# Performance work log

Hardware: AMD Instinct MI355X
Metric: run time of the kernel (lower is better)

The kernel has to match this reference:

```python
import jax, jax.numpy as jnp
import numpy as np

DIM = 384; KEY_DIM = 32; HEADS = 8; ATTN_RATIO = 4; RES = 14
D = ATTN_RATIO * KEY_DIM          # 128
DH = D * HEADS                    # 1024
QK = HEADS * KEY_DIM              # 256
B = 64
EPS = 1e-5
SCALE = KEY_DIM ** -0.5


def _bn(x, p):
    # inference-mode BatchNorm; p = [gamma, beta, mean, var] each [C]; channel axis = 1
    g, b, m, v = p
    shp = (1, -1) + (1,) * (x.ndim - 2)
    return (x - m.reshape(shp)) * jax.lax.rsqrt(v.reshape(shp) + EPS) * g.reshape(shp) + b.reshape(shp)


def _bn_params(k, c):
    k1, k2, k3, k4 = jax.random.split(k, 4)
    gamma = 1.0 + 0.1 * jax.random.normal(k1, (c,), dtype=jnp.float32)
    beta = 0.02 * jax.random.normal(k2, (c,), dtype=jnp.float32)
    mean = 0.1 * jax.random.normal(k3, (c,), dtype=jnp.float32)
    var = jax.random.uniform(k4, (c,), dtype=jnp.float32) + 0.5
    return jnp.stack([gamma, beta, mean, var])


def setup_inputs() -> dict:
    key = jax.random.key(0)
    ks = jax.random.split(key, 24)
    def rn(i, shape, s=0.05):
        return s * jax.random.normal(ks[i], shape, dtype=jnp.float32)
    # relative-position bias index table: offset (|dy|,|dx|) -> dy*RES+dx
    coords = np.stack(np.meshgrid(np.arange(RES), np.arange(RES), indexing='ij'), -1).reshape(-1, 2)
    off = np.abs(coords[:, None, :] - coords[None, :, :])  # [N,N,2]
    bias_idxs = jnp.asarray(off[..., 0] * RES + off[..., 1], dtype=jnp.int32)  # [N,N]
    return {
        'x': jax.random.normal(ks[0], (B, DIM, RES, RES), dtype=jnp.float32),
        'wq': rn(1, (QK, DIM)), 'bq': rn(2, (QK,)), 'bnq': _bn_params(ks[3], QK),
        'wk': rn(4, (QK, DIM)), 'bk': rn(5, (QK,)), 'bnk': _bn_params(ks[6], QK),
        'wv': rn(7, (DH, DIM)), 'bv': rn(8, (DH,)), 'bnv': _bn_params(ks[9], DH),
        'wvl': rn(10, (DH, 1, 3, 3)), 'bvl': rn(11, (DH,)), 'bnvl': _bn_params(ks[12], DH),
        'th1w': rn(13, (HEADS, HEADS), 0.2), 'th1b': rn(14, (HEADS,)),
        'th2w': rn(15, (HEADS, HEADS), 0.2), 'th2b': rn(16, (HEADS,)),
        'wp': rn(17, (DIM, DH)), 'bp': rn(18, (DIM,)), 'bnp': _bn_params(ks[19], DIM),
        'ab': rn(20, (HEADS, RES * RES), 0.1),
        'bias_idxs': bias_idxs,
    }


def reference(x, wq, bq, bnq, wk, bk, bnk, wv, bv, bnv, wvl, bvl, bnvl,
              th1w, th1b, th2w, th2b, wp, bp, bnp, ab, bias_idxs):
    Bn, C, H, W = x.shape
    N = H * W
    xf = x.reshape(Bn, C, N)
    # 1x1 conv + BN branches (channel GEMMs)
    q = _bn(jnp.einsum('oc,bcn->bon', wq, xf) + bq[None, :, None], bnq)
    k = _bn(jnp.einsum('oc,bcn->bon', wk, xf) + bk[None, :, None], bnk)
    v = _bn(jnp.einsum('oc,bcn->bon', wv, xf) + bv[None, :, None], bnv)  # [B,DH,N]
    # local value path: 3x3 depthwise conv + BN
    v_img = v.reshape(Bn, DH, H, W)
    v_local = jax.lax.conv_general_dilated(
        v_img, wvl, window_strides=(1, 1), padding='SAME',
        feature_group_count=DH, dimension_numbers=('NCHW', 'OIHW', 'NCHW'))
    v_local = _bn(v_local + bvl[None, :, None, None], bnvl)
    # attention
    qh = q.reshape(Bn, HEADS, KEY_DIM, N).transpose(0, 1, 3, 2)  # b h n d
    kh = k.reshape(Bn, HEADS, KEY_DIM, N)                        # b h d m
    vh = v.reshape(Bn, HEADS, D, N).transpose(0, 1, 3, 2)        # b h m e
    attn = jnp.einsum('bhnd,bhdm->bhnm', qh, kh) * SCALE
    attn = attn + ab[:, bias_idxs][None]                         # [1,H,N,N] positional bias
    attn = jnp.einsum('oh,bhnm->bonm', th1w, attn) + th1b[None, :, None, None]
    attn = jax.nn.softmax(attn, axis=-1)
    attn = jnp.einsum('oh,bhnm->bonm', th2w, attn) + th2b[None, :, None, None]
    out = jnp.einsum('bhnm,bhme->bhne', attn, vh)                # b h n e
    out = out.transpose(0, 1, 3, 2).reshape(Bn, DH, H, W) + v_local
    # proj: ReLU -> 1x1 conv -> BN
    out = jax.nn.relu(out)
    out = jnp.einsum('oc,bchw->bohw', wp, out) + bp[None, :, None, None]
    return _bn(out, bnp)
```

## Files before the change

kernel.cpp:

```cpp
#include <hip/hip_runtime.h>

#define B_     64
#define DIM_   384
#define RES_   14
#define N_     196
#define HEADS_ 8
#define KD_    32
#define D_     128
#define DH_    1024
#define QK_    256
#define CH_    1536
#define EPS_   1e-5f
#define SCALE_ 0.17677669529663687f

typedef unsigned short u16;
typedef unsigned int u32;
typedef short v8s __attribute__((ext_vector_type(8)));
typedef float v4f __attribute__((ext_vector_type(4)));
typedef u16  v4u __attribute__((ext_vector_type(4)));
typedef u32  v2u __attribute__((ext_vector_type(2)));
typedef _Float16 h2 __attribute__((ext_vector_type(2)));

static __device__ __forceinline__ u16 f2bf(float f) {
    unsigned int u = __builtin_bit_cast(unsigned int, f);
    u = (u + 0x7fffu + ((u >> 16) & 1u)) >> 16;
    return (u16)u;
}
static __device__ __forceinline__ float bf2f(u16 u) {
    unsigned int x = ((unsigned int)u) << 16;
    return __builtin_bit_cast(float, x);
}

#define WBI_OFF  0u
#define WPI_OFF  589824u
#define QI_OFF   983040u
#define KI_OFF   5177344u
#define VI_OFF   9371648u
#define VLOC_U16 53411840u
#define TAIL_OFF 79101952u
#define TB_OFF   98770944u
#define BIASE_OFF 98785920u

template<int KSTEPS>
static __device__ __forceinline__ void gemm_direct(
    const u16* __restrict__ Ag, const u16* __restrict__ Bg,
    v4f acc[4][4], int tid)
{
    const int lane = tid & 63, w = tid >> 6;
    const int wm = (w & 1) * 64, wn = (w >> 1) * 64;
    const int quad = lane >> 4, l16 = lane & 15;
    const u16* pa = Ag + quad * 1024 + (wm + l16) * 8;
    const u16* pb = Bg + quad * 1024 + (wn + l16) * 8;
    v8s a[2][4], b[2][4];
    #pragma unroll
    for (int i = 0; i < 4; i++) {
        a[0][i] = *(const v8s*)(pa + i * 128);
        b[0][i] = *(const v8s*)(pb + i * 128);
    }
    #pragma unroll
    for (int ks = 0; ks < KSTEPS; ks++) {
        const int cur = ks & 1, nxt = cur ^ 1;
        if (ks + 1 < KSTEPS) {
            const u16* qa = pa + (size_t)(ks + 1) * 4096;
            const u16* qb = pb + (size_t)(ks + 1) * 4096;
            #pragma unroll
            for (int i = 0; i < 4; i++) {
                a[nxt][i] = *(const v8s*)(qa + i * 128);
                b[nxt][i] = *(const v8s*)(qb + i * 128);
            }
        }
        #pragma unroll
        for (int i = 0; i < 4; i++)
            #pragma unroll
            for (int j = 0; j < 4; j++)
                acc[i][j] = __builtin_amdgcn_mfma_f32_16x16x32_bf16(a[cur][i], b[cur][j], acc[i][j], 0, 0, 0);
    }
}

template<int KSTEPS>
static __device__ __forceinline__ void gemm_direct3(
    const u16* __restrict__ Ag, const u16* __restrict__ Bg,
    v4f acc[4][4], int tid)
{
    const int lane = tid & 63, w = tid >> 6;
    const int wm = (w & 1) * 64, wn = (w >> 1) * 64;
    const int quad = lane >> 4, l16 = lane & 15;
    const u16* pa = Ag + quad * 1024 + (wm + l16) * 8;
    const u16* pb = Bg + quad * 1024 + (wn + l16) * 8;
    v8s a[3][4], b[3][4];
    #pragma unroll
    for (int s = 0; s < 2; s++) {
        #pragma unroll
        for (int i = 0; i < 4; i++) {
            a[s][i] = *(const v8s*)(pa + (size_t)s * 4096 + i * 128);
            b[s][i] = *(const v8s*)(pb + (size_t)s * 4096 + i * 128);
        }
    }
    #pragma unroll
    for (int ks = 0; ks < KSTEPS; ks++) {
        const int cur = ks % 3, nxt = (ks + 2) % 3;
        if (ks + 2 < KSTEPS) {
            const u16* qa = pa + (size_t)(ks + 2) * 4096;
            const u16* qb = pb + (size_t)(ks + 2) * 4096;
            #pragma unroll
            for (int i = 0; i < 4; i++) {
                a[nxt][i] = *(const v8s*)(qa + i * 128);
                b[nxt][i] = *(const v8s*)(qb + i * 128);
            }
        }
        #pragma unroll
        for (int i = 0; i < 4; i++)
            #pragma unroll
            for (int j = 0; j < 4; j++)
                acc[i][j] = __builtin_amdgcn_mfma_f32_16x16x32_bf16(a[cur][i], b[cur][j], acc[i][j], 0, 0, 0);
    }
}

__global__ __launch_bounds__(256) void k_pre(
    const float* __restrict__ x,
    const float* __restrict__ wq, const float* __restrict__ wk,
    const float* __restrict__ wv, const float* __restrict__ wp,
    const float* __restrict__ ab,
    const float* __restrict__ th1w, const float* __restrict__ th1b,
    const float* __restrict__ bq, const float* __restrict__ bnq,
    const float* __restrict__ bk, const float* __restrict__ bnk,
    const float* __restrict__ bv, const float* __restrict__ bnv,
    const float* __restrict__ bp, const float* __restrict__ bnp,
    const float* __restrict__ bvl, const float* __restrict__ bnvl,
    const int* __restrict__ bidx,
    u16* __restrict__ xI, u16* __restrict__ WbI, u16* __restrict__ WpI,
    float* __restrict__ TB, float* __restrict__ biasE)
{
    __shared__ float T[64][65];
    const int tid = threadIdx.x;
    if (blockIdx.x < 1536) {
        const int t  = blockIdx.x;
        const int n0 = (t & 3) * 64;
        const int k0 = ((t >> 2) % 6) * 64;
        const int b  = t / 24;
        const int c = tid & 63, r4 = tid >> 6;
        #pragma unroll
        for (int i = 0; i < 16; i++) {
            int kr = i * 4 + r4;
            int gn = n0 + c;
            T[kr][c] = (gn < N_) ? x[((size_t)b * DIM_ + k0 + kr) * N_ + gn] : 0.f;
        }
        __syncthreads();
        #pragma unroll
        for (int it = 0; it < 16; it++) {
            int j = it * 256 + tid;
            int kk = j & 63, nn = j >> 6;
            int k = k0 + kk, n = n0 + nn;
            xI[(size_t)b * 98304 + (n >> 7) * 49152 + (k >> 5) * 4096
               + ((k >> 3) & 3) * 1024 + (n & 127) * 8 + (k & 7)] = f2bf(T[kk][nn]);
        }
        return;
    }
    int i = (blockIdx.x - 1536) * 256 + tid;
    if (i < 589824) {
        int mt = i / 49152, rem = i % 49152;
        int ks = rem >> 12, r2 = rem & 4095;
        int q = r2 >> 10, row = (r2 >> 3) & 127, e = r2 & 7;
        int c = mt * 128 + row, k = ks * 32 + q * 8 + e;
        float v = (c < 256) ? wq[c * 384 + k]
                : (c < 512) ? wk[(c - 256) * 384 + k]
                            : wv[(size_t)(c - 512) * 384 + k];
        WbI[i] = f2bf(v);
    } else if (i < 983040) {
        int j = i - 589824;
        int mt = j >> 17, rem = j & 131071;
        int ks = rem >> 12, r2 = rem & 4095;
        int q = r2 >> 10, row = (r2 >> 3) & 127, e = r2 & 7;
        int p = mt * 128 + row, k = ks * 32 + q * 8 + e;
        WpI[j] = f2bf(wp[(size_t)p * 1024 + k]);
    } else if (i < 985984) {
        int j = i - 983040;
        if (j < 256) {
            int c = j;
            float s = bnq[c] * rsqrtf(bnq[768 + c] + EPS_);
            float t = (bq[c] - bnq[512 + c]) * s + bnq[256 + c];
            TB[c] = s * SCALE_; TB[256 + c] = t * SCALE_;
        } else if (j < 512) {
            int c = j - 256;
            float s = bnk[c] * rsqrtf(bnk[768 + c] + EPS_);
            float t = (bk[c] - bnk[512 + c]) * s + bnk[256 + c];
            TB[512 + c] = s; TB[768 + c] = t;
        } else if (j < 1536) {
            int c = j - 512;
            float s = bnv[c] * rsqrtf(bnv[3072 + c] + EPS_);
            float t = (bv[c] - bnv[2048 + c]) * s + bnv[1024 + c];
            TB[1024 + c] = s; TB[2048 + c] = t;
        } else if (j < 1920) {
            int c = j - 1536;
            float s = bnp[c] * rsqrtf(bnp[1152 + c] + EPS_);
            float t = (bp[c] - bnp[768 + c]) * s + bnp[384 + c];
            TB[3072 + c] = s; TB[3456 + c] = t;
        } else {
            int c = j - 1920;
            float s = bnvl[c] * rsqrtf(bnvl[3072 + c] + EPS_);
            float t = (bvl[c] - bnvl[2048 + c]) * s + bnvl[1024 + c];
            TB[3840 + c] = s; TB[4864 + c] = t;
        }
    } else if (i < 1293312) {
        int j = i - 985984;
        int m = j % N_;
        int t = j / N_;
        int o = t & 7;
        int n = t >> 3;
        int idx = bidx[n * N_ + m];
        float a = th1b[o];
        #pragma unroll
        for (int h = 0; h < 8; h++) a += th1w[o * 8 + h] * ab[h * N_ + idx];
        biasE[j] = a - 5.f;
    }
}

__global__ __launch_bounds__(256) void k_qkv(
    const u16* __restrict__ WbI, const u16* __restrict__ xI,
    const float* __restrict__ TB,
    u16* __restrict__ qI, u16* __restrict__ kI, u16* __restrict__ vI)
{
    const int tid = threadIdx.x;
    const int L = blockIdx.x + 2 * (blockIdx.y + 12 * blockIdx.z);
    const int idx = L >> 3;
    const int b  = (L & 7) * 8 + idx / 24;
    const int r  = idx % 24;
    const int mt = r >> 1, nt = r & 1;
    v4f acc[4][4] = {};
    gemm_direct<12>(WbI + (size_t)mt * 49152,
                    xI + ((size_t)b * 2 + nt) * 49152, acc, tid);

    const int lane = tid & 63, w = tid >> 6;
    const int wm = (w & 1) * 64, wn = (w >> 1) * 64;
    const int quad = lane >> 4, l16 = lane & 15;
    #pragma unroll
    for (int i = 0; i < 4; i++) {
        #pragma unroll
        for (int j = 0; j < 4; j++) {
            int gc = mt * 128 + wm + i * 16 + quad * 4;
            int n  = nt * 128 + wn + j * 16 + l16;
            v4f v = acc[i][j];
            if (gc < 256) {
                v4f s = *(const v4f*)&TB[gc];
                v4f t = *(const v4f*)&TB[256 + gc];
                v4u u;
                #pragma unroll
                for (int r2 = 0; r2 < 4; r2++) u[r2] = f2bf(v[r2] * s[r2] + t[r2]);
                *(v4u*)&qI[((size_t)(b * 8 + (gc >> 5)) * 256 + n) * 32 + (gc & 31)] = u;
            } else if (gc < 512) {
                int c = gc - 256;
                v4f s = *(const v4f*)&TB[512 + c];
                v4f t = *(const v4f*)&TB[768 + c];
                v4u u;
                #pragma unroll
                for (int r2 = 0; r2 < 4; r2++) u[r2] = f2bf(v[r2] * s[r2] + t[r2]);
                *(v4u*)&kI[((size_t)(b * 8 + (c >> 5)) * 256 + n) * 32 + (c & 31)] = u;
            } else {
                int c = gc - 512;
                if (n < 224) {
                    int o = c >> 7, e = c & 127;
                    u16* base = vI + ((size_t)(b * 8 + o) * 7 + (n >> 5)) * 4096
                                + ((n >> 3) & 3) * 1024 + (n & 7);
                    #pragma unroll
                    for (int r2 = 0; r2 < 4; r2++) {
                        u16 outv = 0;
                        if (n < N_) outv = f2bf(v[r2] * TB[1024 + c + r2] + TB[2048 + c + r2]);
                        base[(e + r2) * 8] = outv;
                    }
                }
            }
        }
    }
}

__global__ __launch_bounds__(256) void k_dwconv(
    const u16* __restrict__ vI, const float* __restrict__ wvl,
    const float* __restrict__ TB, u16* __restrict__ vlocI)
{
    __shared__ u16 V[64 * 230];
    const int tid = threadIdx.x;
    const int sub = blockIdx.x;
    const int b   = blockIdx.y;
    const int o   = sub >> 1;
    const int e0  = (sub & 1) * 64;
    const u16* img = vI + (size_t)(b * 8 + o) * 28672;

    {
        const int quad = tid >> 6, l = tid & 63;
        #pragma unroll
        for (int i = 0; i < 7; i++) {
            v8s u = *(const v8s*)&img[i * 4096 + quad * 1024 + (e0 + l) * 8];
            const u32* ui = (const u32*)&u;
            int m0 = i * 32 + quad * 8;
            u32* dst = (u32*)&V[l * 230 + m0];
            #pragma unroll
            for (int c = 0; c < 4; c++) dst[c] = ui[c];
        }
    }
    __syncthreads();

    const int e = tid & 63, j = tid >> 6;
    const int cg = sub * 64 + e;
    const int y0 = j * 4;
    const int ny = (j == 3) ? 2 : 4;
    float wgt[9];
    #pragma unroll
    for (int k = 0; k < 9; k++) wgt[k] = wvl[cg * 9 + k];
    const float sc = TB[3840 + cg], sh = TB[4864 + cg];
    u32 po[4][7];

    for (int yi = 0; yi < ny; yi++) {
        int y = y0 + yi;
        float a[3][16];
        #pragma unroll
        for (int dy = 0; dy < 3; dy++) {
            int yy = y + dy - 1;
            a[dy][0] = 0.f; a[dy][15] = 0.f;
            if (yy < 0 || yy > 13) {
                #pragma unroll
                for (int x = 1; x < 15; x++) a[dy][x] = 0.f;
            } else {
                const u16* rp = &V[e * 230 + yy * 14];
                #pragma unroll
                for (int c4 = 0; c4 < 7; c4++) {
                    u32 u = *(const u32*)&rp[c4 * 2];
                    a[dy][1 + 2 * c4] = bf2f((u16)(u & 0xffffu));
                    a[dy][2 + 2 * c4] = bf2f((u16)(u >> 16));
                }
            }
        }
        #pragma unroll
        for (int xp = 0; xp < 7; xp++) {
            u32 pk = 0;
            #pragma unroll
            for (int half = 0; half < 2; half++) {
                int x = 2 * xp + half;
                float s = 0.f;
                #pragma unroll
                for (int dy = 0; dy < 3; dy++)
                    #pragma unroll
                    for (int kx = 0; kx < 3; kx++)
                        s += wgt[dy * 3 + kx] * a[dy][x + kx];
                u16 bv = f2bf(s * sc + sh);
                pk |= ((u32)bv) << (16 * half);
            }
            po[yi][xp] = pk;
        }
    }
    __syncthreads();

    for (int yi = 0; yi < ny; yi++) {
        u32* dst = (u32*)&V[e * 196 + (y0 + yi) * 14];
        #pragma unroll
        for (int xp = 0; xp < 7; xp++) dst[xp] = po[yi][xp];
    }
    __syncthreads();

    for (int it = 0; it < 7; it++) {
        int idx = it * 256 + tid;
        if (idx < 1568) {
            int g = idx / 196, n = idx - g * 196;
            v4u lo, hi;
            #pragma unroll
            for (int r = 0; r < 4; r++) lo[r] = V[(g * 8 + r) * 196 + n];
            #pragma unroll
            for (int r = 0; r < 4; r++) hi[r] = V[(g * 8 + 4 + r) * 196 + n];
            u16* dst = vlocI + ((size_t)(b * 2 + (n >> 7)) * 32 + sub * 2 + (g >> 2)) * 4096
                     + (g & 3) * 1024 + (n & 127) * 8;
            *(v4u*)dst = lo;
            *(v4u*)(dst + 4) = hi;
        }
    }
}

#define SLST 232
__global__ __launch_bounds__(512, 4) void k_attn_av(
    const u16* __restrict__ qI, const u16* __restrict__ kI,
    const u16* __restrict__ vI,
    const float* __restrict__ th1w,
    const float* __restrict__ th2w, const float* __restrict__ th2b,
    const float* __restrict__ biasE,
    const u16* __restrict__ vlocI, u16* __restrict__ aoI)
{
    __shared__ __attribute__((aligned(16))) u16 Ps[2][16 * SLST];
    __shared__ float red[8][8][16];
    __shared__ float invS[8][16];
    __shared__ __attribute__((aligned(16))) u16 Zf[8];
    const int tid = threadIdx.x;
    const int w = tid >> 6, lane = tid & 63;
    const int quad = lane >> 4, l16 = lane & 15;
    const int L = blockIdx.x + 13 * blockIdx.y;
    const int idx = L >> 3;
    const int b  = (L & 7) * 8 + idx / 13;
    const int qt = idx % 13;
    const int n0 = qt * 16;
    if (tid < 8) Zf[tid] = 0;

    const int nmt = (w < 5) ? 2 : 1;
    const int nq  = n0 + l16;
    const int nb  = (nq < N_) ? nq : 0;
    const float* bErow = biasE + (size_t)nb * 1568;

    h2 E[2][8][2] = {};
    #pragma unroll
    for (int mi = 0; mi < 2; mi++) {
        if (mi >= nmt) break;
        const int mt = w + mi * 8;
        v4f S[8];
        const u16* qb0 = qI + (size_t)b * 8 * 8192;
        const u16* kb0 = kI + (size_t)b * 8 * 8192;
        #pragma unroll
        for (int h = 0; h < 8; h++) {
            v8s qf = *(const v8s*)&qb0[h * 8192 + (n0 + l16) * 32 + quad * 8];
            v8s kf = *(const v8s*)&kb0[h * 8192 + (mt * 16 + l16) * 32 + quad * 8];
            v4f z = {};
            S[h] = __builtin_amdgcn_mfma_f32_16x16x32_bf16(kf, qf, z, 0, 0, 0);
        }
        const bool mvalid = (mt < 12) || (quad == 0);
        const int mb = mt * 16 + quad * 4;
        if (mvalid) {
            #pragma unroll
            for (int o = 0; o < 8; o++) {
                v4f a = *(const v4f*)&bErow[o * 196 + mb];
                #pragma unroll
                for (int h = 0; h < 8; h++) {
                    float t1 = th1w[o * 8 + h];
                    #pragma unroll
                    for (int r = 0; r < 4; r++) a[r] += t1 * S[h][r];
                }
                E[mi][o][0] = h2{(_Float16)__expf(a[0]), (_Float16)__expf(a[1])};
                E[mi][o][1] = h2{(_Float16)__expf(a[2]), (_Float16)__expf(a[3])};
            }
        }
    }

    {
        float psum[8];
        #pragma unroll
        for (int o = 0; o < 8; o++) {
            float s = (float)E[0][o][0].x + (float)E[0][o][0].y
                    + (float)E[0][o][1].x + (float)E[0][o][1].y
                    + (float)E[1][o][0].x + (float)E[1][o][0].y
                    + (float)E[1][o][1].x + (float)E[1][o][1].y;
            s += __shfl_xor(s, 16, 64);
            s += __shfl_xor(s, 32, 64);
            psum[o] = s;
        }
        red[w][quad * 2 + 0][l16] = psum[quad * 2 + 0];
        red[w][quad * 2 + 1][l16] = psum[quad * 2 + 1];
    }
    __syncthreads();
    if (tid < 128) {
        int o = tid >> 4, q = tid & 15;
        float s = 0.f;
        #pragma unroll
        for (int wv = 0; wv < 8; wv++) s += red[wv][o][q];
        invS[o][q] = 1.f / s;
    }
    __syncthreads();

    #pragma unroll
    for (int o = 0; o < 8; o++) {
        float is = invS[o][l16];
        h2 is2 = h2{(_Float16)is, (_Float16)is};
        E[0][o][0] *= is2; E[0][o][1] *= is2;
        E[1][o][0] *= is2; E[1][o][1] *= is2;
    }

    const int half_ = n0 >> 7;
    const int row0 = n0 & 127;
    const bool act = (nq < N_);
    char* psrow0 = (char*)&Ps[0][0] + l16 * (SLST * 2);
    char* psrow1 = (char*)&Ps[1][0] + l16 * (SLST * 2);

    #pragma unroll
    for (int o2 = 0; o2 < 8; o2++) {
        char* psb = (o2 & 1) ? psrow1 : psrow0;
        #pragma unroll
        for (int mi = 0; mi < 2; mi++) {
            if (mi >= nmt) break;
            const int mt = w + mi * 8;
            const bool mvalid = (mt < 12) || (quad == 0);
            u32 pk0 = 0, pk1 = 0;
            if (mvalid) {
                float p0 = th2b[o2], p1 = th2b[o2], p2 = th2b[o2], p3 = th2b[o2];
                #pragma unroll
                for (int o = 0; o < 8; o++) {
                    float wgt = th2w[o2 * 8 + o];
                    p0 += wgt * (float)E[mi][o][0].x;
                    p1 += wgt * (float)E[mi][o][0].y;
                    p2 += wgt * (float)E[mi][o][1].x;
                    p3 += wgt * (float)E[mi][o][1].y;
                }
                pk0 = (u32)f2bf(p0) | ((u32)f2bf(p1) << 16);
                pk1 = (u32)f2bf(p2) | ((u32)f2bf(p3) << 16);
            }
            v2u pw; pw[0] = pk0; pw[1] = pk1;
            *(v2u*)(psb + mt * 32 + quad * 8) = pw;
        }
        const u16* vb = vI + (size_t)(b * 8 + o2) * 28672;
        const u16* af = vb + quad * 1024 + (w * 16 + l16) * 8;
        v8s va[7];
        #pragma unroll
        for (int ks = 0; ks < 7; ks++)
            va[ks] = *(const v8s*)(af + (size_t)ks * 4096);
        __syncthreads();

        v4f acc = {};
        __builtin_amdgcn_s_setprio(1);
        #pragma unroll
        for (int ks = 0; ks < 7; ks++) {
            v8s bfr = (ks == 6 && quad >= 2)
                    ? *(const v8s*)&Zf[0]
                    : *(const v8s*)(psb + ks * 64 + quad * 16);
            acc = __builtin_amdgcn_mfma_f32_16x16x32_bf16(va[ks], bfr, acc, 0, 0, 0);
        }
        __builtin_amdgcn_s_setprio(0);

        if (act) {
            const int c0 = o2 * 128 + w * 16 + quad * 4;
            const size_t ioff = ((size_t)(b * 2 + half_) * 32 + (c0 >> 5)) * 4096
                              + ((c0 >> 3) & 3) * 1024 + (size_t)(row0 + l16) * 8 + (c0 & 7);
            v4u lv = *(const v4u*)&vlocI[ioff];
            v4u u;
            #pragma unroll
            for (int r = 0; r < 4; r++)
                u[r] = f2bf(fmaxf(acc[r] + bf2f(lv[r]), 0.f));
            *(v4u*)&aoI[ioff] = u;
        }
    }
}

__global__ __launch_bounds__(256) void k_proj(
    const u16* __restrict__ WpI, const u16* __restrict__ aoI,
    const float* __restrict__ TB, float* __restrict__ out)
{
    const int tid = threadIdx.x;
    const int L = blockIdx.x + 2 * (blockIdx.y + 3 * blockIdx.z);
    const int idx = L >> 3;
    const int b  = (L & 7) * 8 + idx / 6;
    const int r  = idx % 6;
    const int mt = r >> 1, nt = r & 1;
    v4f acc[4][4] = {};
    gemm_direct3<32>(WpI + (size_t)mt * 131072,
                     aoI + ((size_t)b * 2 + nt) * 131072, acc, tid);

    const int lane = tid & 63, w = tid >> 6;
    const int wm = (w & 1) * 64, wn = (w >> 1) * 64;
    const int quad = lane >> 4, l16 = lane & 15;
    #pragma unroll
    for (int i = 0; i < 4; i++) {
        #pragma unroll
        for (int j = 0; j < 4; j++) {
            int p0 = mt * 128 + wm + i * 16 + quad * 4;
            int n  = nt * 128 + wn + j * 16 + l16;
            if (n < N_) {
                v4f s = *(const v4f*)&TB[3072 + p0];
                v4f t = *(const v4f*)&TB[3456 + p0];
                #pragma unroll
                for (int r2 = 0; r2 < 4; r2++)
                    out[((size_t)b * DIM_ + p0 + r2) * N_ + n] = acc[i][j][r2] * s[r2] + t[r2];
            }
        }
    }
}

extern "C" void kernel_launch(void* const* d_in, const int* in_sizes, int n_in,
                              void* d_out, int out_size, void* d_ws, size_t ws_size,
                              hipStream_t stream)
{
    const float* x    = (const float*)d_in[0];
    const float* wq   = (const float*)d_in[1];
    const float* bq   = (const float*)d_in[2];
    const float* bnq  = (const float*)d_in[3];
    const float* wk   = (const float*)d_in[4];
    const float* bk   = (const float*)d_in[5];
    const float* bnk  = (const float*)d_in[6];
    const float* wv   = (const float*)d_in[7];
    const float* bv   = (const float*)d_in[8];
    const float* bnv  = (const float*)d_in[9];
    const float* wvl  = (const float*)d_in[10];
    const float* bvl  = (const float*)d_in[11];
    const float* bnvl = (const float*)d_in[12];
    const float* th1w = (const float*)d_in[13];
    const float* th1b = (const float*)d_in[14];
    const float* th2w = (const float*)d_in[15];
    const float* th2b = (const float*)d_in[16];
    const float* wp   = (const float*)d_in[17];
    const float* bp   = (const float*)d_in[18];
    const float* bnp  = (const float*)d_in[19];
    const float* ab   = (const float*)d_in[20];
    const int*   bidx = (const int*)d_in[21];
    float* out = (float*)d_out;

    u16* wsb  = (u16*)d_ws;
    u16* WbI  = wsb + WBI_OFF;
    u16* WpI  = wsb + WPI_OFF;
    u16* qI   = wsb + QI_OFF;
    u16* kI   = wsb + KI_OFF;
    u16* vI   = wsb + VI_OFF;
    u16* vlocI = wsb + VLOC_U16;
    u16* xI   = wsb + TAIL_OFF;
    u16* aoI  = wsb + TAIL_OFF;
    float* TB    = (float*)(wsb + TB_OFF);
    float* biasE = (float*)(wsb + BIASE_OFF);

    k_pre<<<dim3(6588), 256, 0, stream>>>(x, wq, wk, wv, wp, ab, th1w, th1b,
                                          bq, bnq, bk, bnk, bv, bnv, bp, bnp, bvl, bnvl,
                                          bidx, xI, WbI, WpI, TB, biasE);
    k_qkv<<<dim3(2, 12, B_), 256, 0, stream>>>(WbI, xI, TB, qI, kI, vI);
    k_dwconv<<<dim3(16, B_), 256, 0, stream>>>(vI, wvl, TB, vlocI);
    k_attn_av<<<dim3(13, B_), 512, 0, stream>>>(qI, kI, vI, th1w, th2w, th2b,
                                                biasE, vlocI, aoI);
    k_proj<<<dim3(2, 3, B_), 256, 0, stream>>>(WpI, aoI, TB, out);
}
```

Baseline: 257.1 us.

## Fuse output projection GEMM into attention kernel via shared-memory staging

The separate k_proj launch is removed. Each attention block now stages its ReLU'd bf16 attention output tile (16 queries x 512 channels at a time) in swizzled LDS and multiplies it by Wp with MFMA, accumulating the 384 output channels in registers before applying the final BN affine and writing fp32 output. This drops the aoI round trip through global memory and one kernel launch. In exchange, every block reads all of Wp from global or L2 for only 16 query rows, adds two extra barriers, and uses more LDS and registers, which may reduce occupancy.

```diff
diff --git a/kernel.cpp b/kernel.cpp
--- a/kernel.cpp
+++ b/kernel.cpp
@@ -63,45 +63,6 @@
         if (ks + 1 < KSTEPS) {
             const u16* qa = pa + (size_t)(ks + 1) * 4096;
             const u16* qb = pb + (size_t)(ks + 1) * 4096;
-            #pragma unroll
-            for (int i = 0; i < 4; i++) {
-                a[nxt][i] = *(const v8s*)(qa + i * 128);
-                b[nxt][i] = *(const v8s*)(qb + i * 128);
-            }
-        }
-        #pragma unroll
-        for (int i = 0; i < 4; i++)
-            #pragma unroll
-            for (int j = 0; j < 4; j++)
-                acc[i][j] = __builtin_amdgcn_mfma_f32_16x16x32_bf16(a[cur][i], b[cur][j], acc[i][j], 0, 0, 0);
-    }
-}
-
-template<int KSTEPS>
-static __device__ __forceinline__ void gemm_direct3(
-    const u16* __restrict__ Ag, const u16* __restrict__ Bg,
-    v4f acc[4][4], int tid)
-{
-    const int lane = tid & 63, w = tid >> 6;
-    const int wm = (w & 1) * 64, wn = (w >> 1) * 64;
-    const int quad = lane >> 4, l16 = lane & 15;
-    const u16* pa = Ag + quad * 1024 + (wm + l16) * 8;
-    const u16* pb = Bg + quad * 1024 + (wn + l16) * 8;
-    v8s a[3][4], b[3][4];
-    #pragma unroll
-    for (int s = 0; s < 2; s++) {
-        #pragma unroll
-        for (int i = 0; i < 4; i++) {
-            a[s][i] = *(const v8s*)(pa + (size_t)s * 4096 + i * 128);
-            b[s][i] = *(const v8s*)(pb + (size_t)s * 4096 + i * 128);
-        }
-    }
-    #pragma unroll
-    for (int ks = 0; ks < KSTEPS; ks++) {
-        const int cur = ks % 3, nxt = (ks + 2) % 3;
-        if (ks + 2 < KSTEPS) {
-            const u16* qa = pa + (size_t)(ks + 2) * 4096;
-            const u16* qb = pb + (size_t)(ks + 2) * 4096;
             #pragma unroll
             for (int i = 0; i < 4; i++) {
                 a[nxt][i] = *(const v8s*)(qa + i * 128);
@@ -380,12 +341,15 @@
     const float* __restrict__ th1w,
     const float* __restrict__ th2w, const float* __restrict__ th2b,
     const float* __restrict__ biasE,
-    const u16* __restrict__ vlocI, u16* __restrict__ aoI)
+    const u16* __restrict__ vlocI,
+    const u16* __restrict__ WpI, const float* __restrict__ TB,
+    float* __restrict__ out)
 {
     __shared__ __attribute__((aligned(16))) u16 Ps[2][16 * SLST];
-    __shared__ float red[8][8][16];
-    __shared__ float invS[8][16];
+    __shared__ __attribute__((aligned(16))) u16 Ao[16 * 512];
     __shared__ __attribute__((aligned(16))) u16 Zf[8];
+    float* red  = (float*)&Ao[0];
+    float* invS = (float*)&Ao[2048];
     const int tid = threadIdx.x;
     const int w = tid >> 6, lane = tid & 63;
     const int quad = lane >> 4, l16 = lane & 15;
@@ -446,32 +410,34 @@
             s += __shfl_xor(s, 32, 64);
             psum[o] = s;
         }
-        red[w][quad * 2 + 0][l16] = psum[quad * 2 + 0];
-        red[w][quad * 2 + 1][l16] = psum[quad * 2 + 1];
+        red[(w * 8 + quad * 2 + 0) * 16 + l16] = psum[quad * 2 + 0];
+        red[(w * 8 + quad * 2 + 1) * 16 + l16] = psum[quad * 2 + 1];
     }
     __syncthreads();
     if (tid < 128) {
         int o = tid >> 4, q = tid & 15;
         float s = 0.f;
         #pragma unroll
-        for (int wv = 0; wv < 8; wv++) s += red[wv][o][q];
-        invS[o][q] = 1.f / s;
+        for (int wv = 0; wv < 8; wv++) s += red[(wv * 8 + o) * 16 + q];
+        invS[o * 16 + q] = 1.f / s;
     }
     __syncthreads();
 
     #pragma unroll
     for (int o = 0; o < 8; o++) {
-        float is = invS[o][l16];
+        float is = invS[o * 16 + l16];
         h2 is2 = h2{(_Float16)is, (_Float16)is};
         E[0][o][0] *= is2; E[0][o][1] *= is2;
         E[1][o][0] *= is2; E[1][o][1] *= is2;
     }
 
-    const int half_ = n0 >> 7;
-    const int row0 = n0 & 127;
     const bool act = (nq < N_);
     char* psrow0 = (char*)&Ps[0][0] + l16 * (SLST * 2);
     char* psrow1 = (char*)&Ps[1][0] + l16 * (SLST * 2);
+    char* aorow  = (char*)&Ao[0] + l16 * 1024;
+    const int aswz = (l16 & 7) << 4;
+    const u16* wpb = WpI + quad * 1024 + (w * 16 + l16) * 8;
+    v4f pacc[3] = {};
 
     #pragma unroll
     for (int o2 = 0; o2 < 8; o2++) {
@@ -517,50 +483,49 @@
         }
         __builtin_amdgcn_s_setprio(0);
 
-        if (act) {
-            const int c0 = o2 * 128 + w * 16 + quad * 4;
-            const size_t ioff = ((size_t)(b * 2 + half_) * 32 + (c0 >> 5)) * 4096
-                              + ((c0 >> 3) & 3) * 1024 + (size_t)(row0 + l16) * 8 + (c0 & 7);
-            v4u lv = *(const v4u*)&vlocI[ioff];
-            v4u u;
+        {
+            v4u u = {0, 0, 0, 0};
+            if (act) {
+                const int c0 = o2 * 128 + w * 16 + quad * 4;
+                const size_t ioff = ((size_t)(b * 2 + (n0 >> 7)) * 32 + (c0 >> 5)) * 4096
+                                  + ((c0 >> 3) & 3) * 1024 + (size_t)((n0 & 127) + l16) * 8 + (c0 & 7);
+                v4u lv = *(const v4u*)&vlocI[ioff];
+                #pragma unroll
+                for (int r = 0; r < 4; r++)
+                    u[r] = f2bf(fmaxf(acc[r] + bf2f(lv[r]), 0.f));
+            }
+            const int X = (o2 & 3) * 256 + w * 32 + quad * 8;
+            *(v4u*)(aorow + (X ^ aswz)) = u;
+        }
+
+        if (o2 == 3 || o2 == 7) {
+            __syncthreads();
+            const int kh = o2 >> 2;
+            __builtin_amdgcn_s_setprio(1);
+            #pragma unroll
+            for (int ks = 0; ks < 16; ks++) {
+                v8s bf = *(const v8s*)(aorow + ((ks * 64 + quad * 16) ^ aswz));
+                #pragma unroll
+                for (int t = 0; t < 3; t++) {
+                    v8s a = *(const v8s*)(wpb + (size_t)t * 131072
+                                              + (size_t)(kh * 16 + ks) * 4096);
+                    pacc[t] = __builtin_amdgcn_mfma_f32_16x16x32_bf16(a, bf, pacc[t], 0, 0, 0);
+                }
+            }
+            __builtin_amdgcn_s_setprio(0);
+            if (o2 == 3) __syncthreads();
+        }
+    }
+
+    if (act) {
+        #pragma unroll
+        for (int t = 0; t < 3; t++) {
+            const int p0 = (w + t * 8) * 16 + quad * 4;
+            v4f s = *(const v4f*)&TB[3072 + p0];
+            v4f tt = *(const v4f*)&TB[3456 + p0];
             #pragma unroll
             for (int r = 0; r < 4; r++)
-                u[r] = f2bf(fmaxf(acc[r] + bf2f(lv[r]), 0.f));
-            *(v4u*)&aoI[ioff] = u;
-        }
-    }
-}
-
-__global__ __launch_bounds__(256) void k_proj(
-    const u16* __restrict__ WpI, const u16* __restrict__ aoI,
-    const float* __restrict__ TB, float* __restrict__ out)
-{
-    const int tid = threadIdx.x;
-    const int L = blockIdx.x + 2 * (blockIdx.y + 3 * blockIdx.z);
-    const int idx = L >> 3;
-    const int b  = (L & 7) * 8 + idx / 6;
-    const int r  = idx % 6;
-    const int mt = r >> 1, nt = r & 1;
-    v4f acc[4][4] = {};
-    gemm_direct3<32>(WpI + (size_t)mt * 131072,
-                     aoI + ((size_t)b * 2 + nt) * 131072, acc, tid);
-
-    const int lane = tid & 63, w = tid >> 6;
-    const int wm = (w & 1) * 64, wn = (w >> 1) * 64;
-    const int quad = lane >> 4, l16 = lane & 15;
-    #pragma unroll
-    for (int i = 0; i < 4; i++) {
-        #pragma unroll
-        for (int j = 0; j < 4; j++) {
-            int p0 = mt * 128 + wm + i * 16 + quad * 4;
-            int n  = nt * 128 + wn + j * 16 + l16;
-            if (n < N_) {
-                v4f s = *(const v4f*)&TB[3072 + p0];
-                v4f t = *(const v4f*)&TB[3456 + p0];
-                #pragma unroll
-                for (int r2 = 0; r2 < 4; r2++)
-                    out[((size_t)b * DIM_ + p0 + r2) * N_ + n] = acc[i][j][r2] * s[r2] + t[r2];
-            }
+                out[((size_t)b * DIM_ + p0 + r) * N_ + nq] = pacc[t][r] * s[r] + tt[r];
         }
     }
 }
@@ -601,7 +566,6 @@
     u16* vI   = wsb + VI_OFF;
     u16* vlocI = wsb + VLOC_U16;
     u16* xI   = wsb + TAIL_OFF;
-    u16* aoI  = wsb + TAIL_OFF;
     float* TB    = (float*)(wsb + TB_OFF);
     float* biasE = (float*)(wsb + BIASE_OFF);
 
@@ -611,6 +575,5 @@
     k_qkv<<<dim3(2, 12, B_), 256, 0, stream>>>(WbI, xI, TB, qI, kI, vI);
     k_dwconv<<<dim3(16, B_), 256, 0, stream>>>(vI, wvl, TB, vlocI);
     k_attn_av<<<dim3(13, B_), 512, 0, stream>>>(qI, kI, vI, th1w, th2w, th2b,
-                                                biasE, vlocI, aoI);
-    k_proj<<<dim3(2, 3, B_), 256, 0, stream>>>(WpI, aoI, TB, out);
-}
+                                                biasE, vlocI, WpI, TB, out);
+}
```

Result: slower. 266.8 us (+3.7%).
